# Kernel tuning notes

Measured on AMD Instinct MI355X. Metric: run time of the kernel, lower is better.

The kernel has to match this reference:

```python
import jax, jax.numpy as jnp
import numpy as np
from jax import lax

BITS = 8
STRIDE = 1
PADDING = 1
SCALE = 2.0 ** (BITS - 1)  # fixed-point scale 2^(bits-1)


def setup_inputs() -> dict:
    key = jax.random.key(0)
    k1, k2, k3 = jax.random.split(key, 3)
    x = jax.random.normal(k1, (32, 128, 56, 56), dtype=jnp.float32)
    W = jax.random.normal(k2, (256, 128, 3, 3), dtype=jnp.float32)
    b = jax.random.normal(k3, (256,), dtype=jnp.float32)
    return {"x": x, "W": W, "b": b}


def reference(x, W, b):
    # to_fix_point: round(v * 2^(bits-1)); torch keeps long ints, but all
    # arithmetic in forward promotes back to float, so float round is exact here.
    w_q = jnp.round(W * SCALE)
    b_q = jnp.round(b * SCALE)
    # calConv: out[i,j] = sum(patch * w_q) / 2^(bits-1) + b_q
    # (square 3x3 kernel makes the original's transposed patch indexing a standard conv)
    out = lax.conv_general_dilated(
        x, w_q,
        window_strides=(STRIDE, STRIDE),
        padding=[(PADDING, PADDING), (PADDING, PADDING)],
        dimension_numbers=("NCHW", "OIHW", "NCHW"),
    )
    return out / SCALE + b_q[None, :, None, None]
```

## Files before the change

### kernel.cpp

```cpp
#include <hip/hip_runtime.h>

typedef _Float16 half8 __attribute__((ext_vector_type(8)));
typedef float floatx4 __attribute__((ext_vector_type(4)));

#define IMG   3136
#define PIMG  3364
#define XP_ELEMS (32 * 58 * 58 * 128)
#define WQ_ELEMS (9 * 256 * 128)

#define AS1 __attribute__((address_space(1)))
#define AS3 __attribute__((address_space(3)))

__global__ __launch_bounds__(256) void prep_kernel(const float* __restrict__ x,
                                                   const float* __restrict__ W,
                                                   _Float16* __restrict__ xp,
                                                   _Float16* __restrict__ wq) {
    const int bid = blockIdx.x;
    const int t   = threadIdx.x;
    if (bid >= 1856) {
        int U = (bid - 1856) * 256 + t;
        int l  = U & 63;
        int wv = (U >> 6) & 7;
        int g  = (U >> 9) & 1;
        int h  = (U >> 10) & 1;
        int T  = U >> 11;
        int rs = T >> 1, kt = T & 1;
        int k  = h * 128 + g * 64 + wv * 8 + (l >> 3);
        int c0 = kt * 64 + (((l & 7) ^ ((l >> 3) & 7)) * 8);
        _Float16* d = wq + (long)U * 8;
        #pragma unroll
        for (int j = 0; j < 8; ++j)
            d[j] = (_Float16)rintf(W[(k * 128 + c0 + j) * 9 + rs] * 128.0f);
        return;
    }
    const int hh = bid % 58;
    const int n  = bid / 58;
    _Float16* rowbase = xp + ((long)(n * 58 + hh) * 58) * 128;

    if (hh == 0 || hh == 57) {
        #pragma unroll
        for (int i = 0; i < 4; ++i) {
            int idx = i * 256 + t;
            if (idx < 928) *(half8*)(rowbase + idx * 8) = (half8)(_Float16)0.0f;
        }
        return;
    }

    __shared__ _Float16 tile[128 * 57];
    const int h = hh - 1;

    #pragma unroll
    for (int p = 0; p < 7; ++p) {
        int idx = p * 256 + t;
        int c   = idx / 14;
        int w4  = (idx % 14) * 4;
        const float4 v = *(const float4*)(x + ((long)(n * 128 + c) * 56 + h) * 56 + w4);
        _Float16* d = tile + c * 57 + w4;
        d[0] = (_Float16)v.x; d[1] = (_Float16)v.y;
        d[2] = (_Float16)v.z; d[3] = (_Float16)v.w;
    }
    __syncthreads();

    #pragma unroll
    for (int p = 0; p < 4; ++p) {
        int idx = p * 256 + t;
        if (idx < 896) {
            int ww = idx >> 4;
            int c0 = (idx & 15) * 8;
            half8 v;
            #pragma unroll
            for (int j = 0; j < 8; ++j) v[j] = tile[(c0 + j) * 57 + ww];
            *(half8*)(rowbase + (ww + 1) * 128 + c0) = v;
        }
    }
    if (t < 32) {
        int ww = (t >> 4) ? 57 : 0;
        int c0 = (t & 15) * 8;
        *(half8*)(rowbase + ww * 128 + c0) = (half8)(_Float16)0.0f;
    }
}

__global__ __launch_bounds__(512, 2) void conv_mfma_kernel(
    const _Float16* __restrict__ xp, const _Float16* __restrict__ wq,
    const float* __restrict__ b, float* __restrict__ out)
{
    __shared__ __align__(16) _Float16 smem[65536];

    const int tid = threadIdx.x;
    const int l   = tid & 63;
    const int wv  = tid >> 6;
    const int wp  = wv & 1;
    const int wf  = wv >> 1;
    int bx  = blockIdx.x;
    bx = (bx & 7) * 49 + (bx >> 3);

    const int lr3  = l >> 3;
    const int l7   = l & 7;
    const int l47  = l >> 4;
    const int lswz = ((l & 7) ^ (lr3 & 7)) * 16;

    long pbB[4];
    #pragma unroll
    for (int hg = 0; hg < 4; ++hg) {
        const int pix = bx * 256 + hg * 64 + wv * 8 + lr3;
        const int n = pix / IMG, hw = pix % IMG;
        pbB[hg] = (long)(n * PIMG + (hw / 56) * 58 + (hw % 56)) * 256 + lswz;
    }
    const long abase = (long)wv * 1024 + l * 16;

    floatx4 acc[8][4] = {};

    auto stageA = [&](int T, int h, int pbuf) {
        const char* src = (const char*)wq + (long)((T * 2 + h) * 2) * 8192 + abase;
        _Float16* dst = smem + pbuf * 32768 + (h * 128 + wv * 8) * 64;
        __builtin_amdgcn_global_load_lds((AS1 void*)src,          (AS3 void*)dst,          16, 0, 0);
        __builtin_amdgcn_global_load_lds((AS1 void*)(src + 8192), (AS3 void*)(dst + 4096), 16, 0, 0);
    };
    auto stageB = [&](int T, int h, int pbuf) {
        const int rs = T >> 1, kt = T & 1;
        const int r  = (rs * 11) >> 5;
        const int s2 = rs - r * 3;
        const long toff = (long)(r * 58 + s2) * 256 + kt * 128;
        const char* xb = (const char*)xp + toff;
        _Float16* dst = smem + pbuf * 32768 + 16384 + (h * 128 + wv * 8) * 64;
        __builtin_amdgcn_global_load_lds((AS1 void*)(xb + pbB[h * 2 + 0]), (AS3 void*)dst,          16, 0, 0);
        __builtin_amdgcn_global_load_lds((AS1 void*)(xb + pbB[h * 2 + 1]), (AS3 void*)(dst + 4096), 16, 0, 0);
    };

    const int frow = wf * 64  + (l & 15);
    const int prow = wp * 128 + (l & 15);

    stageB(0, 0, 0); stageB(0, 1, 0); stageA(0, 0, 0); stageA(0, 1, 0);

    #pragma unroll 2
    for (int T = 0; T < 18; ++T) {
        const int pb = T & 1;
        const _Float16* As = smem + pb * 32768;
        const _Float16* Bs = As + 16384;
        if (T < 17) {
            stageB(T + 1, 0, pb ^ 1);
            asm volatile("s_waitcnt vmcnt(2)" ::: "memory");
        } else {
            asm volatile("s_waitcnt vmcnt(0)" ::: "memory");
        }
        asm volatile("s_barrier" ::: "memory");

        half8 ff[4][2], pf[8][2];
        #pragma unroll
        for (int ni = 0; ni < 4; ++ni) {
            ff[ni][0] = *(const half8*)(As + (frow + ni * 16) * 64 + ((0 + l47) ^ l7) * 8);
            ff[ni][1] = *(const half8*)(As + (frow + ni * 16) * 64 + ((4 + l47) ^ l7) * 8);
        }
        #pragma unroll
        for (int mi = 0; mi < 8; ++mi) {
            pf[mi][0] = *(const half8*)(Bs + (prow + mi * 16) * 64 + ((0 + l47) ^ l7) * 8);
            pf[mi][1] = *(const half8*)(Bs + (prow + mi * 16) * 64 + ((4 + l47) ^ l7) * 8);
        }
        if (T < 17) { stageB(T + 1, 1, pb ^ 1); stageA(T + 1, 0, pb ^ 1); stageA(T + 1, 1, pb ^ 1); }

        __builtin_amdgcn_s_setprio(1);
        #pragma unroll
        for (int kk = 0; kk < 2; ++kk)
            #pragma unroll
            for (int mi = 0; mi < 8; ++mi)
                #pragma unroll
                for (int ni = 0; ni < 4; ++ni)
                    acc[mi][ni] = __builtin_amdgcn_mfma_f32_16x16x32_f16(pf[mi][kk], ff[ni][kk], acc[mi][ni], 0, 0, 0);
        __builtin_amdgcn_s_setprio(0);

        asm volatile("s_barrier" ::: "memory");
    }

    #pragma unroll
    for (int mi = 0; mi < 8; ++mi) {
        const int pix = bx * 256 + wp * 128 + mi * 16 + (l >> 4) * 4;
        const int n  = pix / IMG;
        const int pr = pix - n * IMG;
        float* orow = out + (long)n * 256 * IMG + pr;
        #pragma unroll
        for (int ni = 0; ni < 4; ++ni) {
            const int filt = wf * 64 + ni * 16 + (l & 15);
            const float bq = rintf(b[filt] * 128.0f);
            float4 v;
            v.x = acc[mi][ni][0] * (1.0f / 128.0f) + bq;
            v.y = acc[mi][ni][1] * (1.0f / 128.0f) + bq;
            v.z = acc[mi][ni][2] * (1.0f / 128.0f) + bq;
            v.w = acc[mi][ni][3] * (1.0f / 128.0f) + bq;
            *(float4*)(orow + (long)filt * IMG) = v;
        }
    }
}

__global__ void conv_fallback_kernel(const float* __restrict__ x, const float* __restrict__ W,
                                     const float* __restrict__ b, float* __restrict__ out)
{
    __shared__ float wsm[1152];
    const int k = blockIdx.y;
    for (int i = threadIdx.x; i < 1152; i += 256)
        wsm[i] = rintf(W[k * 1152 + i] * 128.0f);
    __syncthreads();
    const int pix = blockIdx.x * 256 + threadIdx.x;
    const int n = pix / IMG, hw = pix % IMG;
    const int h = hw / 56, w = hw % 56;
    float acc = 0.0f;
    for (int c = 0; c < 128; ++c) {
        const float* xr = x + ((n * 128 + c) * 56) * 56;
        const float* wr = wsm + c * 9;
        #pragma unroll
        for (int r = 0; r < 3; ++r) {
            const int hh = h + r - 1;
            if ((unsigned)hh >= 56u) continue;
            #pragma unroll
            for (int s = 0; s < 3; ++s) {
                const int ww = w + s - 1;
                if ((unsigned)ww >= 56u) continue;
                acc += xr[hh * 56 + ww] * wr[r * 3 + s];
            }
        }
    }
    out[((long)n * 256 + k) * IMG + hw] = acc * (1.0f / 128.0f) + rintf(b[k] * 128.0f);
}

extern "C" void kernel_launch(void* const* d_in, const int* in_sizes, int n_in,
                              void* d_out, int out_size, void* d_ws, size_t ws_size,
                              hipStream_t stream) {
    const float* x = (const float*)d_in[0];
    const float* W = (const float*)d_in[1];
    const float* b = (const float*)d_in[2];
    float* out = (float*)d_out;

    const size_t need = (size_t)XP_ELEMS * 2 + (size_t)WQ_ELEMS * 2;
    if (ws_size >= need) {
        _Float16* xp = (_Float16*)d_ws;
        _Float16* wq = xp + XP_ELEMS;
        prep_kernel<<<2000, 256, 0, stream>>>(x, W, xp, wq);
        conv_mfma_kernel<<<dim3(392), 512, 0, stream>>>(xp, wq, b, out);
    } else {
        conv_fallback_kernel<<<dim3(392, 256), 256, 0, stream>>>(x, W, b, out);
    }
}
```

Measured before the change: 208.5 us.

## Load weight fragments directly from global into registers, shrink LDS tiles

The weight operand is now read by each wave straight from global memory into registers in MFMA fragment order, instead of being staged through LDS. The prep kernel repacks the quantized weights to match that order. Only the activation operand still goes through LDS, now in 32-channel K-steps (36 steps) with a new XOR swizzle, which cuts shared memory from 128KB to 32KB per block and could raise occupancy. The cost is twice as many barrier-synchronized iterations, each with less MFMA work, plus per-wave global weight loads that depend on L1/L2 hits.

```diff
diff --git a/kernel.cpp b/kernel.cpp
--- a/kernel.cpp
+++ b/kernel.cpp
@@ -18,15 +18,14 @@
     const int bid = blockIdx.x;
     const int t   = threadIdx.x;
     if (bid >= 1856) {
-        int U = (bid - 1856) * 256 + t;
+        int U  = (bid - 1856) * 256 + t;
         int l  = U & 63;
-        int wv = (U >> 6) & 7;
-        int g  = (U >> 9) & 1;
-        int h  = (U >> 10) & 1;
-        int T  = U >> 11;
-        int rs = T >> 1, kt = T & 1;
-        int k  = h * 128 + g * 64 + wv * 8 + (l >> 3);
-        int c0 = kt * 64 + (((l & 7) ^ ((l >> 3) & 7)) * 8);
+        int ni = (U >> 6) & 3;
+        int wf = (U >> 8) & 3;
+        int s  = U >> 10;
+        int rs = s >> 2, cc = s & 3;
+        int k  = wf * 64 + ni * 16 + (l & 15);
+        int c0 = cc * 32 + (l >> 4) * 8;
         _Float16* d = wq + (long)U * 8;
         #pragma unroll
         for (int j = 0; j < 8; ++j)
@@ -84,7 +83,7 @@
     const _Float16* __restrict__ xp, const _Float16* __restrict__ wq,
     const float* __restrict__ b, float* __restrict__ out)
 {
-    __shared__ __align__(16) _Float16 smem[65536];
+    __shared__ __align__(16) _Float16 smem[16384];
 
     const int tid = threadIdx.x;
     const int l   = tid & 63;
@@ -94,81 +93,65 @@
     int bx  = blockIdx.x;
     bx = (bx & 7) * 49 + (bx >> 3);
 
-    const int lr3  = l >> 3;
-    const int l7   = l & 7;
-    const int l47  = l >> 4;
-    const int lswz = ((l & 7) ^ (lr3 & 7)) * 16;
-
-    long pbB[4];
-    #pragma unroll
-    for (int hg = 0; hg < 4; ++hg) {
-        const int pix = bx * 256 + hg * 64 + wv * 8 + lr3;
+    long pbB[2];
+    #pragma unroll
+    for (int h = 0; h < 2; ++h) {
+        const int pix = bx * 256 + h * 128 + wv * 16 + (l >> 2);
         const int n = pix / IMG, hw = pix % IMG;
-        pbB[hg] = (long)(n * PIMG + (hw / 56) * 58 + (hw % 56)) * 256 + lswz;
-    }
-    const long abase = (long)wv * 1024 + l * 16;
+        pbB[h] = (long)(n * PIMG + (hw / 56) * 58 + (hw % 56)) * 256
+               + ((l & 3) ^ ((l >> 3) & 3)) * 16;
+    }
+    const int kq = ((l >> 4) ^ ((l >> 1) & 3)) * 8;
 
     floatx4 acc[8][4] = {};
 
-    auto stageA = [&](int T, int h, int pbuf) {
-        const char* src = (const char*)wq + (long)((T * 2 + h) * 2) * 8192 + abase;
-        _Float16* dst = smem + pbuf * 32768 + (h * 128 + wv * 8) * 64;
-        __builtin_amdgcn_global_load_lds((AS1 void*)src,          (AS3 void*)dst,          16, 0, 0);
-        __builtin_amdgcn_global_load_lds((AS1 void*)(src + 8192), (AS3 void*)(dst + 4096), 16, 0, 0);
-    };
-    auto stageB = [&](int T, int h, int pbuf) {
-        const int rs = T >> 1, kt = T & 1;
+    auto stageB = [&](int s, int pbuf) {
+        const int rs = s >> 2;
+        const int cc = s & 3;
         const int r  = (rs * 11) >> 5;
         const int s2 = rs - r * 3;
-        const long toff = (long)(r * 58 + s2) * 256 + kt * 128;
+        const long toff = (long)(r * 58 + s2) * 256 + cc * 64;
         const char* xb = (const char*)xp + toff;
-        _Float16* dst = smem + pbuf * 32768 + 16384 + (h * 128 + wv * 8) * 64;
-        __builtin_amdgcn_global_load_lds((AS1 void*)(xb + pbB[h * 2 + 0]), (AS3 void*)dst,          16, 0, 0);
-        __builtin_amdgcn_global_load_lds((AS1 void*)(xb + pbB[h * 2 + 1]), (AS3 void*)(dst + 4096), 16, 0, 0);
+        _Float16* dst = smem + pbuf * 8192 + wv * 512;
+        __builtin_amdgcn_global_load_lds((AS1 void*)(xb + pbB[0]), (AS3 void*)dst,          16, 0, 0);
+        __builtin_amdgcn_global_load_lds((AS1 void*)(xb + pbB[1]), (AS3 void*)(dst + 4096), 16, 0, 0);
     };
-
-    const int frow = wf * 64  + (l & 15);
-    const int prow = wp * 128 + (l & 15);
-
-    stageB(0, 0, 0); stageB(0, 1, 0); stageA(0, 0, 0); stageA(0, 1, 0);
-
-    #pragma unroll 2
-    for (int T = 0; T < 18; ++T) {
-        const int pb = T & 1;
-        const _Float16* As = smem + pb * 32768;
-        const _Float16* Bs = As + 16384;
-        if (T < 17) {
-            stageB(T + 1, 0, pb ^ 1);
-            asm volatile("s_waitcnt vmcnt(2)" ::: "memory");
+    auto loadA = [&](int s, half8 (&ff)[4]) {
+        const char* base = (const char*)wq + (long)(s * 16 + wf * 4) * 1024 + l * 16;
+        #pragma unroll
+        for (int ni = 0; ni < 4; ++ni)
+            ff[ni] = *(const half8*)(base + ni * 1024);
+    };
+
+    auto body = [&](int s, half8 (&ffC)[4], half8 (&ffN)[4]) {
+        const int pb = s & 1;
+        if (s < 35) {
+            loadA(s + 1, ffN);
+            stageB(s + 1, pb ^ 1);
+            asm volatile("s_waitcnt vmcnt(6)" ::: "memory");
         } else {
             asm volatile("s_waitcnt vmcnt(0)" ::: "memory");
         }
         asm volatile("s_barrier" ::: "memory");
-
-        half8 ff[4][2], pf[8][2];
-        #pragma unroll
-        for (int ni = 0; ni < 4; ++ni) {
-            ff[ni][0] = *(const half8*)(As + (frow + ni * 16) * 64 + ((0 + l47) ^ l7) * 8);
-            ff[ni][1] = *(const half8*)(As + (frow + ni * 16) * 64 + ((4 + l47) ^ l7) * 8);
-        }
+        const _Float16* Bs = smem + pb * 8192;
+        __builtin_amdgcn_s_setprio(1);
         #pragma unroll
         for (int mi = 0; mi < 8; ++mi) {
-            pf[mi][0] = *(const half8*)(Bs + (prow + mi * 16) * 64 + ((0 + l47) ^ l7) * 8);
-            pf[mi][1] = *(const half8*)(Bs + (prow + mi * 16) * 64 + ((4 + l47) ^ l7) * 8);
-        }
-        if (T < 17) { stageB(T + 1, 1, pb ^ 1); stageA(T + 1, 0, pb ^ 1); stageA(T + 1, 1, pb ^ 1); }
-
-        __builtin_amdgcn_s_setprio(1);
-        #pragma unroll
-        for (int kk = 0; kk < 2; ++kk)
+            const half8 pf = *(const half8*)(Bs + (wp * 128 + mi * 16 + (l & 15)) * 32 + kq);
             #pragma unroll
-            for (int mi = 0; mi < 8; ++mi)
-                #pragma unroll
-                for (int ni = 0; ni < 4; ++ni)
-                    acc[mi][ni] = __builtin_amdgcn_mfma_f32_16x16x32_f16(pf[mi][kk], ff[ni][kk], acc[mi][ni], 0, 0, 0);
+            for (int ni = 0; ni < 4; ++ni)
+                acc[mi][ni] = __builtin_amdgcn_mfma_f32_16x16x32_f16(pf, ffC[ni], acc[mi][ni], 0, 0, 0);
+        }
         __builtin_amdgcn_s_setprio(0);
-
         asm volatile("s_barrier" ::: "memory");
+    };
+
+    half8 ffA[4], ffB[4];
+    loadA(0, ffA);
+    stageB(0, 0);
+    for (int sp = 0; sp < 18; ++sp) {
+        body(2 * sp,     ffA, ffB);
+        body(2 * sp + 1, ffB, ffA);
     }
 
     #pragma unroll
```

New measurement: 226.5 us. 8.6% more time.
